# Kernel tuning notes

Hardware: AMD Instinct MI355X
Metric: run time of the kernel (lower is better)

The kernel has to match this reference:

```python
import jax, jax.numpy as jnp
import numpy as np

B, SQ, SKV = 4, 2048, 2048
INPUT_DIM, EMBED_DIM, NUM_HEADS = 1024, 1024, 16
HEAD_DIM = EMBED_DIM // NUM_HEADS


def setup_inputs() -> dict:
    key = jax.random.key(0)
    kq, kc, kwkv, kwo = jax.random.split(key, 4)
    # xavier-uniform style scale for weights
    def xavier(k, shape):
        fan_in, fan_out = shape
        lim = jnp.sqrt(6.0 / (fan_in + fan_out))
        return jax.random.uniform(k, shape, jnp.float32, -lim, lim)
    return {
        "q": jax.random.normal(kq, (B, SQ, EMBED_DIM), jnp.float32),
        "c": jax.random.normal(kc, (B, SKV, INPUT_DIM), jnp.float32),
        "W_kv": xavier(kwkv, (INPUT_DIM, 2 * EMBED_DIM)),
        "b_kv": jnp.zeros((2 * EMBED_DIM,), jnp.float32),
        "W_o": xavier(kwo, (EMBED_DIM, EMBED_DIM)),
        "b_o": jnp.zeros((EMBED_DIM,), jnp.float32),
    }


def reference(q, c, W_kv, b_kv, W_o, b_o):
    Bc, Skv, _ = c.shape
    Bq, Sq, embed_dim = q.shape
    # KV projection from context: [B, Skv, 2*embed_dim]
    kv = c @ W_kv + b_kv
    kv = kv.reshape(Bc, Skv, NUM_HEADS, 2 * HEAD_DIM).transpose(0, 2, 1, 3)  # [B,H,Skv,2*hd]
    k, v = jnp.split(kv, 2, axis=-1)  # each [B,H,Skv,hd]
    # q is pre-projected; just split into heads
    qh = q.reshape(Bq, Sq, NUM_HEADS, HEAD_DIM).transpose(0, 2, 1, 3)  # [B,H,Sq,hd]
    scale = 1.0 / jnp.sqrt(jnp.asarray(HEAD_DIM, q.dtype))
    logits = jnp.einsum("bhqd,bhkd->bhqk", qh, k) * scale  # [B,H,Sq,Skv]
    attn = jax.nn.softmax(logits, axis=-1)
    values = jnp.einsum("bhqk,bhkd->bhqd", attn, v)  # [B,H,Sq,hd]
    values = values.transpose(0, 2, 1, 3).reshape(Bc, Sq, embed_dim)
    out = values @ W_o + b_o
    return out
```

## Files before the change

kernel.cpp:

```cpp
#include <hip/hip_runtime.h>

typedef __bf16 bf16x8 __attribute__((ext_vector_type(8)));
typedef float f32x4 __attribute__((ext_vector_type(4)));
typedef unsigned short u16;
typedef unsigned short u16x4 __attribute__((ext_vector_type(4)));
typedef unsigned short u16x8 __attribute__((ext_vector_type(8)));

#define DEVFN __device__ __forceinline__

DEVFN u16 f32_to_bf16(float f) {
  unsigned int u = __float_as_uint(f);
  u += 0x7FFFu + ((u >> 16) & 1u);
  return (u16)(u >> 16);
}

DEVFN u16 f32_to_bf16_fast(float f) {
  return (u16)((__float_as_uint(f) + 0x8000u) >> 16);
}

DEVFN void load_lds16(const void* g, void* l) {
  __builtin_amdgcn_global_load_lds(
      (__attribute__((address_space(1))) void*)g,
      (__attribute__((address_space(3))) void*)l,
      16, 0, 0);
}

__global__ void cvt_cq_kernel(const float* __restrict__ c, const float* __restrict__ q,
                              u16* __restrict__ c_bf, u16* __restrict__ qh) {
  const int bid = blockIdx.x;
  if (bid < 4096) {
    int i = bid * 256 + threadIdx.x;
    const float4* p = (const float4*)c + (size_t)i * 2;
    float4 a = p[0], b = p[1];
    u16x8 o;
    o[0] = f32_to_bf16(a.x); o[1] = f32_to_bf16(a.y);
    o[2] = f32_to_bf16(a.z); o[3] = f32_to_bf16(a.w);
    o[4] = f32_to_bf16(b.x); o[5] = f32_to_bf16(b.y);
    o[6] = f32_to_bf16(b.z); o[7] = f32_to_bf16(b.w);
    *(u16x8*)(c_bf + (size_t)i * 8) = o;
  } else {
    const float SC = 0.125f * 1.44269504088896f;
    int i = (bid - 4096) * 256 + threadIdx.x;
    int dc = i & 7, sx = (i >> 3) & 2047, h = (i >> 14) & 15, b = i >> 18;
    const float4* p = (const float4*)(q + ((size_t)(b * 2048 + sx)) * 1024 + h * 64 + dc * 8);
    float4 a = p[0], bb = p[1];
    u16x8 o;
    o[0] = f32_to_bf16(a.x * SC);  o[1] = f32_to_bf16(a.y * SC);
    o[2] = f32_to_bf16(a.z * SC);  o[3] = f32_to_bf16(a.w * SC);
    o[4] = f32_to_bf16(bb.x * SC); o[5] = f32_to_bf16(bb.y * SC);
    o[6] = f32_to_bf16(bb.z * SC); o[7] = f32_to_bf16(bb.w * SC);
    *(u16x8*)(qh + (size_t)i * 8) = o;
  }
}

__global__ void transpose_w_kernel(const float* __restrict__ in, u16* __restrict__ out, int N) {
  __shared__ __align__(16) u16 T[64 * 72];
  const int tid = threadIdx.x;
  const int n0 = blockIdx.x * 64, k0 = blockIdx.y * 64;
#pragma unroll
  for (int p = 0; p < 4; ++p) {
    int l = p * 256 + tid;
    int k = l >> 4, nc = l & 15;
    const float4 v = *(const float4*)(in + (size_t)(k0 + k) * N + n0 + nc * 4);
    T[(nc * 4 + 0) * 72 + k] = f32_to_bf16(v.x);
    T[(nc * 4 + 1) * 72 + k] = f32_to_bf16(v.y);
    T[(nc * 4 + 2) * 72 + k] = f32_to_bf16(v.z);
    T[(nc * 4 + 3) * 72 + k] = f32_to_bf16(v.w);
  }
  __syncthreads();
#pragma unroll
  for (int p = 0; p < 2; ++p) {
    int u = p * 256 + tid;
    int n = u >> 3, kc = u & 7;
    u16x8 o = *(const u16x8*)(T + n * 72 + kc * 8);
    *(u16x8*)(out + (size_t)(n0 + n) * 1024 + k0 + kc * 8) = o;
  }
}

template <int MODE>
__global__ __launch_bounds__(256, 2) void gemm128(
    const u16* __restrict__ A, const u16* __restrict__ Bt,
    const float* __restrict__ bias,
    u16* __restrict__ outK, u16* __restrict__ outV,
    float* __restrict__ outF, int K) {
  __shared__ __align__(16) u16 SMEM[2 * 128 * 64];
  u16* As = SMEM;
  u16* Bs = SMEM + 128 * 64;
  const int tid = threadIdx.x;
  const int lane = tid & 63, w = tid >> 6, quad = lane >> 4, l15 = lane & 15;
  const int wm = w & 1, wn = w >> 1;
  const int tn = blockIdx.x, tm = blockIdx.y;
  const u16* Ab = A + (size_t)tm * 128 * K;
  const u16* Bb = Bt + (size_t)tn * 128 * K;

  const f32x4 zero4 = {0.f, 0.f, 0.f, 0.f};
  f32x4 acc[4][4];
#pragma unroll
  for (int mi = 0; mi < 4; ++mi)
#pragma unroll
    for (int ni = 0; ni < 4; ++ni) acc[mi][ni] = zero4;

  for (int k0 = 0; k0 < K; k0 += 64) {
#pragma unroll
    for (int p = 0; p < 4; ++p) {
      int l = p * 256 + tid;
      int r = l >> 3, dc = l & 7;
      int go = r * K + k0 + ((dc ^ (r & 7)) * 8);
      int lb = (p * 256 + (tid & 192)) * 8;
      load_lds16(Ab + go, As + lb);
      load_lds16(Bb + go, Bs + lb);
    }
    __syncthreads();
#pragma unroll
    for (int kk = 0; kk < 2; ++kk) {
      bf16x8 av[4], bv[4];
#pragma unroll
      for (int i = 0; i < 4; ++i) {
        int sw = ((kk * 4 + quad) ^ (l15 & 7)) * 8;
        av[i] = *(const bf16x8*)(As + (wm * 64 + i * 16 + l15) * 64 + sw);
        bv[i] = *(const bf16x8*)(Bs + (wn * 64 + i * 16 + l15) * 64 + sw);
      }
#pragma unroll
      for (int mi = 0; mi < 4; ++mi)
#pragma unroll
        for (int ni = 0; ni < 4; ++ni)
          acc[mi][ni] = __builtin_amdgcn_mfma_f32_16x16x32_bf16(av[mi], bv[ni], acc[mi][ni], 0, 0, 0);
    }
    __syncthreads();
  }

  if (MODE == 0) {
    const int h = tn;
    const int b = tm >> 4;
    const int sx0 = (tm & 15) * 128;
    u16* VT = SMEM;
    if (wn == 0) {
#pragma unroll
      for (int ni = 0; ni < 4; ++ni) {
        const int d = ni * 16 + l15;
        const float bb = bias[tn * 128 + d];
#pragma unroll
        for (int mi = 0; mi < 4; ++mi) {
#pragma unroll
          for (int r = 0; r < 4; ++r) {
            const int sx = sx0 + wm * 64 + mi * 16 + quad * 4 + r;
            outK[((size_t)(b * 16 + h) * 2048 + sx) * 64 + d] = f32_to_bf16(acc[mi][ni][r] + bb);
          }
        }
      }
    } else {
#pragma unroll
      for (int ni = 0; ni < 4; ++ni) {
        const int d = ni * 16 + l15;
        const float bb = bias[tn * 128 + 64 + d];
#pragma unroll
        for (int mi = 0; mi < 4; ++mi) {
          u16x4 pk;
#pragma unroll
          for (int r = 0; r < 4; ++r) pk[r] = f32_to_bf16(acc[mi][ni][r] + bb);
          *(u16x4*)(VT + d * 136 + wm * 64 + mi * 16 + quad * 4) = pk;
        }
      }
    }
    __syncthreads();
    {
      const int d = tid >> 2, ch = tid & 3;
      u16* dst = outV + (((size_t)(b * 16 + h) * 64 + d) * 2048 + sx0 + ch * 32);
      const u16* src = VT + d * 136 + ch * 32;
#pragma unroll
      for (int i = 0; i < 4; ++i)
        *(u16x8*)(dst + i * 8) = *(const u16x8*)(src + i * 8);
    }
  } else {
#pragma unroll
    for (int ni = 0; ni < 4; ++ni) {
      const int n = tn * 128 + wn * 64 + ni * 16 + l15;
      const float bb = bias[n];
#pragma unroll
      for (int mi = 0; mi < 4; ++mi) {
#pragma unroll
        for (int r = 0; r < 4; ++r) {
          const int m = tm * 128 + wm * 64 + mi * 16 + quad * 4 + r;
          outF[(size_t)m * 1024 + n] = acc[mi][ni][r] + bb;
        }
      }
    }
  }
}

#define PSTR 40

__global__ __launch_bounds__(256, 4) void flash_kernel(
    const u16* __restrict__ Qh,
    const u16* __restrict__ Kp,
    const u16* __restrict__ Vt,
    u16* __restrict__ Opk) {
  __shared__ __align__(16) u16 Ks[128 * 64];
  __shared__ __align__(16) u16 Vts[64 * 128];
  __shared__ __align__(16) u16 Ps[4][16 * PSTR];
  __shared__ float lbuf[4][16];

  const int tid = threadIdx.x;
  const int lane = tid & 63, w = tid >> 6, quad = lane >> 4, l15 = lane & 15;
  const int id = blockIdx.x;
  const int bh = (id & 7) + 8 * (id >> 8);
  const int qt = (id >> 3) & 31;
  const int q0 = qt * 64;

  const u16* kbase = Kp + (size_t)bh * 2048 * 64;
  const u16* vbase = Vt + (size_t)bh * 64 * 2048;

  const u16* qrow = Qh + ((size_t)bh * 2048 + q0 + w * 16 + l15) * 64;
  bf16x8 bq0 = *(const bf16x8*)(qrow + quad * 8);
  bf16x8 bq1 = *(const bf16x8*)(qrow + 32 + quad * 8);

  const f32x4 zero4 = {0.f, 0.f, 0.f, 0.f};
  f32x4 oacc[4];
  f32x4 lsumv = zero4;
#pragma unroll
  for (int di = 0; di < 4; ++di) oacc[di] = zero4;

  u16* myP = &Ps[w][0];

  for (int t = 0; t < 16; ++t) {
    const int kv0 = t * 128;
#pragma unroll
    for (int p = 0; p < 4; ++p) {
      int l = p * 256 + tid;
      int kv = l >> 3, dc = l & 7;
      load_lds16(kbase + (kv0 + kv) * 64 + ((dc ^ (kv & 7)) * 8), Ks + (p * 256 + (tid & 192)) * 8);
    }
#pragma unroll
    for (int p = 0; p < 4; ++p) {
      int l = p * 256 + tid;
      int d = l >> 4, dc = l & 15;
      load_lds16(vbase + (size_t)d * 2048 + kv0 + ((dc ^ (d & 15)) * 8),
                 Vts + (p * 256 + (tid & 192)) * 8);
    }
    __syncthreads();

#pragma unroll
    for (int c = 0; c < 4; ++c) {
      f32x4 s0 = zero4, s1 = zero4;
      {
        const int sw0 = (quad ^ (l15 & 7)) * 8;
        bf16x8 ak0 = *(const bf16x8*)(Ks + ((c * 2 + 0) * 16 + l15) * 64 + sw0);
        bf16x8 ak1 = *(const bf16x8*)(Ks + ((c * 2 + 1) * 16 + l15) * 64 + sw0);
        s0 = __builtin_amdgcn_mfma_f32_16x16x32_bf16(ak0, bq0, s0, 0, 0, 0);
        s1 = __builtin_amdgcn_mfma_f32_16x16x32_bf16(ak1, bq0, s1, 0, 0, 0);
        const int sw1 = ((4 + quad) ^ (l15 & 7)) * 8;
        ak0 = *(const bf16x8*)(Ks + ((c * 2 + 0) * 16 + l15) * 64 + sw1);
        ak1 = *(const bf16x8*)(Ks + ((c * 2 + 1) * 16 + l15) * 64 + sw1);
        s0 = __builtin_amdgcn_mfma_f32_16x16x32_bf16(ak0, bq1, s0, 0, 0, 0);
        s1 = __builtin_amdgcn_mfma_f32_16x16x32_bf16(ak1, bq1, s1, 0, 0, 0);
      }

#pragma unroll
      for (int k2 = 0; k2 < 2; ++k2) {
        const f32x4& s = (k2 == 0) ? s0 : s1;
        u16x4 pk;
        f32x4 pv;
#pragma unroll
        for (int r = 0; r < 4; ++r) {
          pv[r] = __builtin_amdgcn_exp2f(s[r]);
          pk[r] = f32_to_bf16_fast(pv[r]);
        }
        lsumv += pv;
        *(u16x4*)(myP + l15 * PSTR + k2 * 16 + quad * 4) = pk;
      }

      bf16x8 ap = *(const bf16x8*)(myP + l15 * PSTR + quad * 8);
#pragma unroll
      for (int di = 0; di < 4; ++di) {
        bf16x8 bv = *(const bf16x8*)(Vts + (di * 16 + l15) * 128 + (((c * 4 + quad) ^ l15) * 8));
        oacc[di] = __builtin_amdgcn_mfma_f32_16x16x32_bf16(ap, bv, oacc[di], 0, 0, 0);
      }
    }
    __syncthreads();
  }

  {
    float v = lsumv[0] + lsumv[1] + lsumv[2] + lsumv[3];
    v += __shfl_xor(v, 16);
    v += __shfl_xor(v, 32);
    if (lane < 16) lbuf[w][lane] = v;
  }

  const int b = bh >> 4, h = bh & 15;
#pragma unroll
  for (int r = 0; r < 4; ++r) {
    float linv = 1.0f / lbuf[w][quad * 4 + r];
    int row = q0 + w * 16 + quad * 4 + r;
    u16* dst = Opk + ((size_t)(b * 2048 + row)) * 1024 + h * 64;
#pragma unroll
    for (int di = 0; di < 4; ++di)
      dst[di * 16 + l15] = f32_to_bf16(oacc[di][r] * linv);
  }
}


extern "C" void kernel_launch(void* const* d_in, const int* in_sizes, int n_in,
                              void* d_out, int out_size, void* d_ws, size_t ws_size,
                              hipStream_t stream) {
  const float* q   = (const float*)d_in[0];
  const float* c   = (const float*)d_in[1];
  const float* Wkv = (const float*)d_in[2];
  const float* bkv = (const float*)d_in[3];
  const float* Wo  = (const float*)d_in[4];
  const float* bo  = (const float*)d_in[5];
  float* out = (float*)d_out;
  char* ws = (char*)d_ws;

  u16* c_bf = (u16*)(ws + 0);
  u16* qh   = (u16*)(ws + 16777216);
  u16* Wkvt = (u16*)(ws + 33554432);
  u16* Wot  = (u16*)(ws + 37748736);
  u16* KpB  = (u16*)(ws + 39845888);
  u16* VtB  = (u16*)(ws + 56623104);
  u16* Opk  = c_bf;

  cvt_cq_kernel<<<8192, 256, 0, stream>>>(c, q, c_bf, qh);
  transpose_w_kernel<<<dim3(32, 16), 256, 0, stream>>>(Wkv, Wkvt, 2048);
  transpose_w_kernel<<<dim3(16, 16), 256, 0, stream>>>(Wo, Wot, 1024);
  gemm128<0><<<dim3(16, 64), 256, 0, stream>>>(c_bf, Wkvt, bkv, KpB, VtB, nullptr, 1024);
  flash_kernel<<<2048, 256, 0, stream>>>(qh, KpB, VtB, Opk);
  gemm128<1><<<dim3(8, 64), 256, 0, stream>>>(Opk, Wot, bo, nullptr, nullptr, out, 1024);
}
```

Baseline: 305.2 us.

## Redistribute softmax probabilities in registers via permlane swaps instead of LDS

The flash kernel no longer round-trips the bf16 probability tile through a per-wave LDS buffer. It packs pairs of probabilities with v_cvt_pk_bf16_f32 and reshuffles them across lanes using permlane32/permlane16 swaps to build the MFMA A operand directly. The row-sum exchange also moves from LDS to shuffles, and occupancy is raised to 5 blocks. This removes LDS writes and reads plus their latency from the inner loop. It relies on the gfx950 permlane swap layout matching the MFMA operand order, and it switches the conversion to round-to-nearest-even.

```diff
diff --git a/kernel.cpp b/kernel.cpp
--- a/kernel.cpp
+++ b/kernel.cpp
@@ -5,6 +5,7 @@
 typedef unsigned short u16;
 typedef unsigned short u16x4 __attribute__((ext_vector_type(4)));
 typedef unsigned short u16x8 __attribute__((ext_vector_type(8)));
+typedef unsigned int u32x2 __attribute__((ext_vector_type(2)));
 
 #define DEVFN __device__ __forceinline__
 
@@ -14,8 +15,10 @@
   return (u16)(u >> 16);
 }
 
-DEVFN u16 f32_to_bf16_fast(float f) {
-  return (u16)((__float_as_uint(f) + 0x8000u) >> 16);
+DEVFN unsigned int cvt_pk_bf16(float a, float b) {
+  unsigned int r;
+  asm("v_cvt_pk_bf16_f32 %0, %1, %2" : "=v"(r) : "v"(a), "v"(b));
+  return r;
 }
 
 DEVFN void load_lds16(const void* g, void* l) {
@@ -188,17 +191,13 @@
   }
 }
 
-#define PSTR 40
-
-__global__ __launch_bounds__(256, 4) void flash_kernel(
+__global__ __launch_bounds__(256, 5) void flash_kernel(
     const u16* __restrict__ Qh,
     const u16* __restrict__ Kp,
     const u16* __restrict__ Vt,
     u16* __restrict__ Opk) {
   __shared__ __align__(16) u16 Ks[128 * 64];
   __shared__ __align__(16) u16 Vts[64 * 128];
-  __shared__ __align__(16) u16 Ps[4][16 * PSTR];
-  __shared__ float lbuf[4][16];
 
   const int tid = threadIdx.x;
   const int lane = tid & 63, w = tid >> 6, quad = lane >> 4, l15 = lane & 15;
@@ -219,8 +218,6 @@
   f32x4 lsumv = zero4;
 #pragma unroll
   for (int di = 0; di < 4; ++di) oacc[di] = zero4;
-
-  u16* myP = &Ps[w][0];
 
   for (int t = 0; t < 16; ++t) {
     const int kv0 = t * 128;
@@ -255,21 +252,31 @@
         s1 = __builtin_amdgcn_mfma_f32_16x16x32_bf16(ak1, bq1, s1, 0, 0, 0);
       }
 
-#pragma unroll
-      for (int k2 = 0; k2 < 2; ++k2) {
-        const f32x4& s = (k2 == 0) ? s0 : s1;
-        u16x4 pk;
-        f32x4 pv;
-#pragma unroll
-        for (int r = 0; r < 4; ++r) {
-          pv[r] = __builtin_amdgcn_exp2f(s[r]);
-          pk[r] = f32_to_bf16_fast(pv[r]);
-        }
-        lsumv += pv;
-        *(u16x4*)(myP + l15 * PSTR + k2 * 16 + quad * 4) = pk;
-      }
-
-      bf16x8 ap = *(const bf16x8*)(myP + l15 * PSTR + quad * 8);
+      f32x4 pv0, pv1;
+#pragma unroll
+      for (int r = 0; r < 4; ++r) {
+        pv0[r] = __builtin_amdgcn_exp2f(s0[r]);
+        pv1[r] = __builtin_amdgcn_exp2f(s1[r]);
+      }
+      lsumv += pv0;
+      lsumv += pv1;
+      unsigned int a0 = cvt_pk_bf16(pv0[0], pv0[1]);
+      unsigned int a1 = cvt_pk_bf16(pv0[2], pv0[3]);
+      unsigned int b0 = cvt_pk_bf16(pv1[0], pv1[1]);
+      unsigned int b1 = cvt_pk_bf16(pv1[2], pv1[3]);
+
+      u32x2 t0 = __builtin_amdgcn_permlane32_swap(a0, b0, false, false);
+      u32x2 t1 = __builtin_amdgcn_permlane32_swap(a1, b1, false, false);
+      u32x2 u0 = __builtin_amdgcn_permlane16_swap(t0.x, t0.y, false, false);
+      u32x2 u1 = __builtin_amdgcn_permlane16_swap(t1.x, t1.y, false, false);
+
+      union { unsigned int u[4]; bf16x8 v; } P;
+      P.u[0] = u0.x;
+      P.u[1] = u1.x;
+      P.u[2] = u0.y;
+      P.u[3] = u1.y;
+      bf16x8 ap = P.v;
+
 #pragma unroll
       for (int di = 0; di < 4; ++di) {
         bf16x8 bv = *(const bf16x8*)(Vts + (di * 16 + l15) * 128 + (((c * 4 + quad) ^ l15) * 8));
@@ -279,17 +286,18 @@
     __syncthreads();
   }
 
+  float lv;
   {
     float v = lsumv[0] + lsumv[1] + lsumv[2] + lsumv[3];
     v += __shfl_xor(v, 16);
     v += __shfl_xor(v, 32);
-    if (lane < 16) lbuf[w][lane] = v;
+    lv = v;
   }
 
   const int b = bh >> 4, h = bh & 15;
 #pragma unroll
   for (int r = 0; r < 4; ++r) {
-    float linv = 1.0f / lbuf[w][quad * 4 + r];
+    float linv = 1.0f / __shfl(lv, quad * 4 + r);
     int row = q0 + w * 16 + quad * 4 + r;
     u16* dst = Opk + ((size_t)(b * 2048 + row)) * 1024 + h * 64;
 #pragma unroll
```

Measured after the change: 287.6 us. 1.06x faster.
